# Performance work log

Hardware: AMD Instinct MI355X
Metric: run time of the kernel (lower is better)

Reference implementation:

```python
import jax, jax.numpy as jnp
import numpy as np


def setup_inputs() -> dict:
    key = jax.random.key(0)
    k1, k2 = jax.random.split(key)
    H = W = 4096
    input1 = jax.random.normal(k1, (1, 1, H, W), dtype=jnp.float32)   # moving image
    input2 = jax.random.normal(k2, (1, 2, H, W), dtype=jnp.float32)   # dense flow (dH, dW)
    return {"input1": input1, "input2": input2}


def reference(input1, input2):
    # input1: [B=1, C=1, H, W] image; input2: [B=1, 2, H, W] displacement field
    B, C, H, W = input1.shape
    f32 = jnp.float32

    # identity mesh (matches torch.linspace outer-product construction)
    h_mesh = jnp.broadcast_to(jnp.arange(H, dtype=f32)[None, :, None], (B, H, W))
    w_mesh = jnp.broadcast_to(jnp.arange(W, dtype=f32)[None, None, :], (B, H, W))

    # warped sampling coordinates, shifted by +1 for the zero-padding border
    H_up = (input2[:, 0] + h_mesh).reshape(-1) + 1.0   # [B*H*W]
    W_up = (input2[:, 1] + w_mesh).reshape(-1) + 1.0

    # zero-pad image by 1 pixel on each spatial side
    img = jnp.pad(input1, ((0, 0), (0, 0), (1, 1), (1, 1)))  # [B, C, H+2, W+2]
    Hp, Wp = H + 2, W + 2

    hf = jnp.floor(H_up).astype(jnp.int32)
    hc = hf + 1
    wf = jnp.floor(W_up).astype(jnp.int32)
    wc = wf + 1
    hf = jnp.clip(hf, 0, Hp - 1)
    hc = jnp.clip(hc, 0, Hp - 1)
    wf = jnp.clip(wf, 0, Wp - 1)
    wc = jnp.clip(wc, 0, Wp - 1)

    img_flat = img.reshape(-1)  # B = C = 1
    val_000 = img_flat[hf * Wp + wf]
    val_010 = img_flat[hc * Wp + wf]
    val_001 = img_flat[hf * Wp + wc]
    val_011 = img_flat[hc * Wp + wc]

    dH = hc.astype(f32) - H_up
    dW = wc.astype(f32) - W_up
    out = (val_000 * (dW * dH)
           + val_010 * (dW * (1.0 - dH))
           + val_001 * ((1.0 - dW) * dH)
           + val_011 * ((1.0 - dW) * (1.0 - dH)))

    # [B*H*W] -> [B, H, W, C] -> [B, C, H, W]
    return out.reshape(B, H, W, C).transpose(0, 3, 1, 2)
```

## Files before the change

### kernel.cpp

```cpp
#include <hip/hip_runtime.h>


#define IMG_H 4096
#define IMG_W 4096

__global__ __launch_bounds__(256) void warp_bilinear_kernel(
    const float* __restrict__ img,
    const float* __restrict__ flow,
    float* __restrict__ out)
{
    const int HW   = IMG_H * IMG_W;
    const int lane = threadIdx.x & 63;
    const int wv   = threadIdx.x >> 6;
    const int w    = blockIdx.x * 64 + lane;
    const int h0   = blockIdx.y * 16 + wv;

    int   idx[4];
    float fh[4], fw[4];

    #pragma unroll
    for (int k = 0; k < 4; ++k)
        idx[k] = (h0 + 4 * k) * IMG_W + w;

    #pragma unroll
    for (int k = 0; k < 4; ++k)
        fh[k] = __builtin_nontemporal_load(flow + idx[k]);
    #pragma unroll
    for (int k = 0; k < 4; ++k)
        fw[k] = __builtin_nontemporal_load(flow + HW + idx[k]);

    int   o00[4], o10[4], o01[4], o11[4];
    float w00[4], w10[4], w01[4], w11[4];

    #pragma unroll
    for (int k = 0; k < 4; ++k) {
        const int h = h0 + 4 * k;
        float Hu = (fh[k] + (float)h) + 1.0f;
        float Wu = (fw[k] + (float)w) + 1.0f;

        int hf = (int)floorf(Hu);
        int wf = (int)floorf(Wu);
        int hc = hf + 1;
        int wc = wf + 1;

        int hfc = min(max(hf, 0), IMG_H + 1);
        int hcc = min(max(hc, 0), IMG_H + 1);
        int wfc = min(max(wf, 0), IMG_W + 1);
        int wcc = min(max(wc, 0), IMG_W + 1);

        float dH = (float)hcc - Hu;
        float dW = (float)wcc - Wu;

        int rf = hfc - 1, rc = hcc - 1, cf = wfc - 1, cc = wcc - 1;
        bool rf_in = (unsigned)rf < IMG_H;
        bool rc_in = (unsigned)rc < IMG_H;
        bool cf_in = (unsigned)cf < IMG_W;
        bool cc_in = (unsigned)cc < IMG_W;
        int rf_cl = min(max(rf, 0), IMG_H - 1);
        int rc_cl = min(max(rc, 0), IMG_H - 1);
        int cf_cl = min(max(cf, 0), IMG_W - 1);
        int cc_cl = min(max(cc, 0), IMG_W - 1);

        o00[k] = (rf_cl << 12) + cf_cl;
        o10[k] = (rc_cl << 12) + cf_cl;
        o01[k] = (rf_cl << 12) + cc_cl;
        o11[k] = (rc_cl << 12) + cc_cl;

        float A = dW * dH;
        float B = dW * (1.0f - dH);
        float C = (1.0f - dW) * dH;
        float D = (1.0f - dW) * (1.0f - dH);
        w00[k] = (rf_in && cf_in) ? A : 0.0f;
        w10[k] = (rc_in && cf_in) ? B : 0.0f;
        w01[k] = (rf_in && cc_in) ? C : 0.0f;
        w11[k] = (rc_in && cc_in) ? D : 0.0f;
    }

    float v00[4], v10[4], v01[4], v11[4];
    #pragma unroll
    for (int k = 0; k < 4; ++k) {
        v00[k] = img[o00[k]];
        v10[k] = img[o10[k]];
        v01[k] = img[o01[k]];
        v11[k] = img[o11[k]];
    }

    #pragma unroll
    for (int k = 0; k < 4; ++k) {
        float res = v00[k] * w00[k] + v10[k] * w10[k]
                  + v01[k] * w01[k] + v11[k] * w11[k];
        __builtin_nontemporal_store(res, out + idx[k]);
    }
}

extern "C" void kernel_launch(void* const* d_in, const int* in_sizes, int n_in,
                              void* d_out, int out_size, void* d_ws, size_t ws_size,
                              hipStream_t stream) {
    const float* img  = (const float*)d_in[0];
    const float* flow = (const float*)d_in[1];
    float* out = (float*)d_out;

    dim3 grid(IMG_W / 64, IMG_H / 16);
    dim3 block(256);
    warp_bilinear_kernel<<<grid, block, 0, stream>>>(img, flow, out);
}
```

Before: 254.9 us.

## Vectorize flow/output I/O and fetch bilinear taps as float2 pairs

Each thread now handles a 2x2 pixel patch, so flow loads and output stores become 8-byte float2 accesses. The four image gathers per pixel shrink to two unaligned float2 loads, one per row, starting at a clamped base column. Weights are redistributed onto the x/y slots of each pair so that border clamping stays correct. This cuts the number of gather and load/store instructions, in exchange for extra select arithmetic and possibly misaligned 8-byte loads.

```diff
diff --git a/kernel.cpp b/kernel.cpp
--- a/kernel.cpp
+++ b/kernel.cpp
@@ -3,6 +3,9 @@
 
 #define IMG_H 4096
 #define IMG_W 4096
+
+typedef float f2  __attribute__((ext_vector_type(2)));
+typedef float f2u __attribute__((ext_vector_type(2), aligned(4)));
 
 __global__ __launch_bounds__(256) void warp_bilinear_kernel(
     const float* __restrict__ img,
@@ -12,84 +15,99 @@
     const int HW   = IMG_H * IMG_W;
     const int lane = threadIdx.x & 63;
     const int wv   = threadIdx.x >> 6;
-    const int w    = blockIdx.x * 64 + lane;
-    const int h0   = blockIdx.y * 16 + wv;
+    const int w0   = blockIdx.x * 128 + lane * 2;
+    const int h0   = blockIdx.y * 8 + wv * 2;
 
-    int   idx[4];
-    float fh[4], fw[4];
+    int rowidx[2];
+    rowidx[0] = h0 * IMG_W + w0;
+    rowidx[1] = rowidx[0] + IMG_W;
+
+    f2 fh[2], fw[2];
+    #pragma unroll
+    for (int r = 0; r < 2; ++r)
+        fh[r] = __builtin_nontemporal_load((const f2*)(flow + rowidx[r]));
+    #pragma unroll
+    for (int r = 0; r < 2; ++r)
+        fw[r] = __builtin_nontemporal_load((const f2*)(flow + HW + rowidx[r]));
+
+    int   o0[2][2], o1[2][2];
+    float a0x[2][2], a0y[2][2], a1x[2][2], a1y[2][2];
 
     #pragma unroll
-    for (int k = 0; k < 4; ++k)
-        idx[k] = (h0 + 4 * k) * IMG_W + w;
+    for (int r = 0; r < 2; ++r) {
+        #pragma unroll
+        for (int c = 0; c < 2; ++c) {
+            const int h = h0 + r;
+            const int w = w0 + c;
+            float Hu = (fh[r][c] + (float)h) + 1.0f;
+            float Wu = (fw[r][c] + (float)w) + 1.0f;
 
-    #pragma unroll
-    for (int k = 0; k < 4; ++k)
-        fh[k] = __builtin_nontemporal_load(flow + idx[k]);
-    #pragma unroll
-    for (int k = 0; k < 4; ++k)
-        fw[k] = __builtin_nontemporal_load(flow + HW + idx[k]);
+            int hf = (int)floorf(Hu);
+            int wf = (int)floorf(Wu);
+            int hc = hf + 1;
+            int wc = wf + 1;
 
-    int   o00[4], o10[4], o01[4], o11[4];
-    float w00[4], w10[4], w01[4], w11[4];
+            int hfc = min(max(hf, 0), IMG_H + 1);
+            int hcc = min(max(hc, 0), IMG_H + 1);
+            int wfc = min(max(wf, 0), IMG_W + 1);
+            int wcc = min(max(wc, 0), IMG_W + 1);
 
-    #pragma unroll
-    for (int k = 0; k < 4; ++k) {
-        const int h = h0 + 4 * k;
-        float Hu = (fh[k] + (float)h) + 1.0f;
-        float Wu = (fw[k] + (float)w) + 1.0f;
+            float dH = (float)hcc - Hu;
+            float dW = (float)wcc - Wu;
 
-        int hf = (int)floorf(Hu);
-        int wf = (int)floorf(Wu);
-        int hc = hf + 1;
-        int wc = wf + 1;
+            int rf = hfc - 1, rc = hcc - 1, cf = wfc - 1, cc = wcc - 1;
+            bool rf_in = (unsigned)rf < IMG_H;
+            bool rc_in = (unsigned)rc < IMG_H;
+            bool cf_in = (unsigned)cf < IMG_W;
+            bool cc_in = (unsigned)cc < IMG_W;
 
-        int hfc = min(max(hf, 0), IMG_H + 1);
-        int hcc = min(max(hc, 0), IMG_H + 1);
-        int wfc = min(max(wf, 0), IMG_W + 1);
-        int wcc = min(max(wc, 0), IMG_W + 1);
+            int rf_cl = min(max(rf, 0), IMG_H - 1);
+            int rc_cl = min(max(rc, 0), IMG_H - 1);
+            int cf_cl = min(max(cf, 0), IMG_W - 1);
+            int cc_cl = min(max(cc, 0), IMG_W - 1);
+            int cb    = min(max(cf, 0), IMG_W - 2);
 
-        float dH = (float)hcc - Hu;
-        float dW = (float)wcc - Wu;
+            int sf = cf_cl - cb;
+            int sc = cc_cl - cb;
 
-        int rf = hfc - 1, rc = hcc - 1, cf = wfc - 1, cc = wcc - 1;
-        bool rf_in = (unsigned)rf < IMG_H;
-        bool rc_in = (unsigned)rc < IMG_H;
-        bool cf_in = (unsigned)cf < IMG_W;
-        bool cc_in = (unsigned)cc < IMG_W;
-        int rf_cl = min(max(rf, 0), IMG_H - 1);
-        int rc_cl = min(max(rc, 0), IMG_H - 1);
-        int cf_cl = min(max(cf, 0), IMG_W - 1);
-        int cc_cl = min(max(cc, 0), IMG_W - 1);
+            o0[r][c] = (rf_cl << 12) + cb;
+            o1[r][c] = (rc_cl << 12) + cb;
 
-        o00[k] = (rf_cl << 12) + cf_cl;
-        o10[k] = (rc_cl << 12) + cf_cl;
-        o01[k] = (rf_cl << 12) + cc_cl;
-        o11[k] = (rc_cl << 12) + cc_cl;
+            float A = dW * dH;
+            float B = dW * (1.0f - dH);
+            float C = (1.0f - dW) * dH;
+            float D = (1.0f - dW) * (1.0f - dH);
+            float w00 = (rf_in && cf_in) ? A : 0.0f;
+            float w10 = (rc_in && cf_in) ? B : 0.0f;
+            float w01 = (rf_in && cc_in) ? C : 0.0f;
+            float w11 = (rc_in && cc_in) ? D : 0.0f;
 
-        float A = dW * dH;
-        float B = dW * (1.0f - dH);
-        float C = (1.0f - dW) * dH;
-        float D = (1.0f - dW) * (1.0f - dH);
-        w00[k] = (rf_in && cf_in) ? A : 0.0f;
-        w10[k] = (rc_in && cf_in) ? B : 0.0f;
-        w01[k] = (rf_in && cc_in) ? C : 0.0f;
-        w11[k] = (rc_in && cc_in) ? D : 0.0f;
+            a0x[r][c] = (sf ? 0.0f : w00) + (sc ? 0.0f : w01);
+            a0y[r][c] = (sf ? w00 : 0.0f) + (sc ? w01 : 0.0f);
+            a1x[r][c] = (sf ? 0.0f : w10) + (sc ? 0.0f : w11);
+            a1y[r][c] = (sf ? w10 : 0.0f) + (sc ? w11 : 0.0f);
+        }
     }
 
-    float v00[4], v10[4], v01[4], v11[4];
+    f2u p0[2][2], p1[2][2];
     #pragma unroll
-    for (int k = 0; k < 4; ++k) {
-        v00[k] = img[o00[k]];
-        v10[k] = img[o10[k]];
-        v01[k] = img[o01[k]];
-        v11[k] = img[o11[k]];
+    for (int r = 0; r < 2; ++r) {
+        #pragma unroll
+        for (int c = 0; c < 2; ++c) {
+            p0[r][c] = *(const f2u*)(img + o0[r][c]);
+            p1[r][c] = *(const f2u*)(img + o1[r][c]);
+        }
     }
 
     #pragma unroll
-    for (int k = 0; k < 4; ++k) {
-        float res = v00[k] * w00[k] + v10[k] * w10[k]
-                  + v01[k] * w01[k] + v11[k] * w11[k];
-        __builtin_nontemporal_store(res, out + idx[k]);
+    for (int r = 0; r < 2; ++r) {
+        f2 res;
+        #pragma unroll
+        for (int c = 0; c < 2; ++c) {
+            res[c] = p0[r][c].x * a0x[r][c] + p0[r][c].y * a0y[r][c]
+                   + p1[r][c].x * a1x[r][c] + p1[r][c].y * a1y[r][c];
+        }
+        __builtin_nontemporal_store(res, (f2*)(out + rowidx[r]));
     }
 }
 
@@ -100,7 +118,7 @@
     const float* flow = (const float*)d_in[1];
     float* out = (float*)d_out;
 
-    dim3 grid(IMG_W / 64, IMG_H / 16);
+    dim3 grid(IMG_W / 128, IMG_H / 8);
     dim3 block(256);
     warp_bilinear_kernel<<<grid, block, 0, stream>>>(img, flow, out);
 }
```

Measured after the change: 243.6 us. -4.5%, faster.
